# Optimization experiments

Measured on AMD Instinct MI355X. Metric: run time of the kernel, lower is better.

The kernel has to match this reference:

```python
import jax, jax.numpy as jnp
import numpy as np

D = 768
H = 12
DH = 64
S = 1500
SCALE = 0.125  # 1/sqrt(64)


def setup_inputs() -> dict:
    key = jax.random.key(0)
    ks = jax.random.split(key, 8)
    def w(k):
        return jax.random.normal(k, (D, D), dtype=jnp.float32) * (1.0 / np.sqrt(D))
    x = jax.random.normal(ks[0], (8, S, D), dtype=jnp.float32)
    return {
        "x": x,
        "Wq": w(ks[1]), "bq": jax.random.normal(ks[2], (D,), dtype=jnp.float32) * 0.02,
        "Wk": w(ks[3]),
        "Wv": w(ks[4]), "bv": jax.random.normal(ks[5], (D,), dtype=jnp.float32) * 0.02,
        "Wo": w(ks[6]), "bo": jax.random.normal(ks[7], (D,), dtype=jnp.float32) * 0.02,
    }


def reference(x, Wq, bq, Wk, Wv, bv, Wo, bo):
    B = x.shape[0]
    # torch Linear: y = x @ W.T + b
    q = (jnp.einsum('bsd,ed->bse', x, Wq) + bq) * SCALE
    k = jnp.einsum('bsd,ed->bse', x, Wk)
    v = jnp.einsum('bsd,ed->bse', x, Wv) + bv
    # split heads: [B, S, H, DH] -> [B, H, S, DH]
    q = q.reshape(B, S, H, DH).transpose(0, 2, 1, 3)
    k = k.reshape(B, S, H, DH).transpose(0, 2, 1, 3)
    v = v.reshape(B, S, H, DH).transpose(0, 2, 1, 3)
    scores = jnp.einsum('bhqd,bhkd->bhqk', q, k)  # [B, H, S, S]
    probs = jax.nn.softmax(scores, axis=-1)
    ctx = jnp.einsum('bhqk,bhkd->bhqd', probs, v)
    ctx = ctx.transpose(0, 2, 1, 3).reshape(B, S, D)
    return jnp.einsum('bsd,ed->bse', ctx, Wo) + bo
```

## Files before the change

kernel.cpp:

```cpp
#include <hip/hip_runtime.h>
#include <hip/hip_bf16.h>

constexpr int kD  = 768;
constexpr int kH  = 12;
constexpr int kDH = 64;
constexpr int kS  = 1500;
constexpr int kSP = 1504;
constexpr int kB  = 8;
constexpr int kM  = kB * kS;
constexpr float kScale = 0.125f;
constexpr int kPSTR = 72;
constexpr int kNK = kD / 32;

typedef __bf16 bf16;
typedef __bf16 bf16x4 __attribute__((ext_vector_type(4)));
typedef __bf16 bf16x8 __attribute__((ext_vector_type(8)));
typedef float  floatx4 __attribute__((ext_vector_type(4)));

__global__ __launch_bounds__(256) void detect_kernel(const void* __restrict__ xraw,
                                                     int* __restrict__ flag) {
    __shared__ int bad;
    if (threadIdx.x == 0) bad = 0;
    __syncthreads();
    const bf16* xb = (const bf16*)xraw;
    int c = 0;
    for (int k = 0; k < 16; k++) {
        int idx = 2 * (threadIdx.x + 256 * k);
        float v = fabsf((float)xb[idx]);
        if (!(v == 0.0f || (v > 1e-20f && v < 1e6f))) c++;
    }
    atomicAdd(&bad, c);
    __syncthreads();
    if (threadIdx.x == 0) *flag = (bad > 8) ? 1 : 0;
}

__global__ __launch_bounds__(256) void cvt_bf16_kernel(const void* __restrict__ src,
                                                       bf16* __restrict__ dst, int n,
                                                       const int* __restrict__ flag) {
    int i = blockIdx.x * 256 + threadIdx.x;
    if (i < n) {
        if (*flag)
            dst[i] = (bf16)((const float*)src)[i];
        else
            dst[i] = ((const bf16*)src)[i];
    }
}

__global__ __launch_bounds__(256) void cvt_f32_kernel(const void* __restrict__ src,
                                                      float* __restrict__ dst, int n,
                                                      const int* __restrict__ flag) {
    int i = blockIdx.x * 256 + threadIdx.x;
    if (i < n) {
        if (*flag)
            dst[i] = ((const float*)src)[i];
        else
            dst[i] = (float)((const bf16*)src)[i];
    }
}

__global__ __launch_bounds__(256) void zeropad_kernel(bf16* __restrict__ q_ws,
                                                      bf16* __restrict__ k_ws,
                                                      bf16* __restrict__ vt_ws) {
    int t = blockIdx.x * 256 + threadIdx.x;
    if (t < kB * kH * (kSP - kS) * kDH) {
        int bh  = t >> 8;
        int rem = t & 255;
        int s   = kS + (rem >> 6);
        int dh  = rem & 63;
        size_t qi = ((size_t)bh * kSP + s) * kDH + dh;
        q_ws[qi] = (bf16)0.f;
        k_ws[qi] = (bf16)0.f;
        size_t vi = ((size_t)bh * kDH + dh) * kSP + s;
        vt_ws[vi] = (bf16)0.f;
    }
}

__device__ __forceinline__ void async_copy16(const bf16* g, bf16* l) {
    __builtin_amdgcn_global_load_lds(
        (const __attribute__((address_space(1))) void*)g,
        (__attribute__((address_space(3))) void*)l,
        16, 0, 0);
}

#define G_STAGE(KK, SB)                                                         \
    {                                                                           \
        const int k0_ = (KK) * 32;                                              \
        async_copy16(gA + k0_, Asm + (SB) * 4096 + wof);                        \
        async_copy16(gA + (size_t)64 * kD + k0_, Asm + (SB) * 4096 + wof + 2048); \
        async_copy16(gB + k0_, Bsm + (SB) * 4096 + wof);                        \
        async_copy16(gB + (size_t)64 * kD + k0_, Bsm + (SB) * 4096 + wof + 2048); \
    }

#define G_COMPUTE(CB)                                                           \
    {                                                                           \
        const bf16* A_ = Asm + (CB) * 4096;                                     \
        const bf16* B_ = Bsm + (CB) * 4096;                                     \
        bf16x8 af[4], bfr[4];                                                   \
        _Pragma("unroll") for (int i = 0; i < 4; i++)                           \
            af[i] = *(const bf16x8*)(A_ + ((wm + i * 16 + lrow) << 5) + (lq << 3)); \
        _Pragma("unroll") for (int j = 0; j < 4; j++)                           \
            bfr[j] = *(const bf16x8*)(B_ + ((wn + j * 16 + lrow) << 5) + (lq << 3)); \
        _Pragma("unroll") for (int i = 0; i < 4; i++)                           \
            _Pragma("unroll") for (int j = 0; j < 4; j++)                       \
                acc[i][j] = __builtin_amdgcn_mfma_f32_16x16x32_bf16(            \
                    af[i], bfr[j], acc[i][j], 0, 0, 0);                         \
    }

#define G_STEP(KK, CB, SB)                                                      \
    {                                                                           \
        if ((KK) + 3 < kNK) G_STAGE((KK) + 3, SB);                              \
        G_COMPUTE(CB);                                                          \
        if ((KK) + 1 < kNK) {                                                   \
            if ((KK) + 3 < kNK) {                                               \
                asm volatile("s_waitcnt vmcnt(8)" ::: "memory");                \
            } else if ((KK) + 2 < kNK) {                                        \
                asm volatile("s_waitcnt vmcnt(4)" ::: "memory");                \
            } else {                                                            \
                asm volatile("s_waitcnt vmcnt(0)" ::: "memory");                \
            }                                                                   \
            __builtin_amdgcn_s_barrier();                                       \
            __builtin_amdgcn_sched_barrier(0);                                  \
        }                                                                       \
    }

__device__ __forceinline__ void gemm128_qb(const bf16* __restrict__ X,
                                           const bf16* __restrict__ W,
                                           int m0, int n0,
                                           bf16* Asm, bf16* Bsm,
                                           floatx4 acc[4][4]) {
    const int tid  = threadIdx.x;
    const int lane = tid & 63;
    const int w    = tid >> 6;
    const int srow = (w << 4) + (lane >> 2);
    const int scol = (lane & 3) << 3;
    const int lrow = lane & 15;
    const int lq   = lane >> 4;
    const int wm   = (w >> 1) << 6;
    const int wn   = (w & 1) << 6;

    const bf16* gA = X + (size_t)(m0 + srow) * kD + scol;
    const bf16* gB = W + (size_t)(n0 + srow) * kD + scol;
    const int wof = w << 9;

    G_STAGE(0, 0);
    G_STAGE(1, 1);
    G_STAGE(2, 2);
    asm volatile("s_waitcnt vmcnt(8)" ::: "memory");
    __builtin_amdgcn_s_barrier();
    __builtin_amdgcn_sched_barrier(0);

#pragma unroll
    for (int ks = 0; ks < kNK; ks += 4) {
        G_STEP(ks,     0, 3);
        G_STEP(ks + 1, 1, 0);
        G_STEP(ks + 2, 2, 1);
        G_STEP(ks + 3, 3, 2);
    }
}

__global__ __launch_bounds__(256) void qkv_kernel(const bf16* __restrict__ X,
                                                  const bf16* __restrict__ Wq,
                                                  const bf16* __restrict__ Wk,
                                                  const bf16* __restrict__ Wv,
                                                  const float* __restrict__ bq,
                                                  const float* __restrict__ bv,
                                                  bf16* __restrict__ q_ws,
                                                  bf16* __restrict__ k_ws,
                                                  bf16* __restrict__ vt_ws) {
    __shared__ bf16 Asm[4 * 4096];
    __shared__ bf16 Bsm[4 * 4096];

    const int lin = blockIdx.x;
    const int wk  = (lin & 7) * 212 + (lin >> 3);
    if (wk >= 94 * 18) return;
    const int bx  = wk / 18;
    const int r   = wk - bx * 18;
    const int m0  = bx << 7;
    const int mat = r / 6;
    const int n0  = (r % 6) << 7;
    const bf16* W = (mat == 0) ? Wq : (mat == 1) ? Wk : Wv;

    floatx4 acc[4][4] = {};
    gemm128_qb(X, W, m0, n0, Asm, Bsm, acc);

    const int tid  = threadIdx.x;
    const int lane = tid & 63;
    const int w    = tid >> 6;
    const int lrow = lane & 15;
    const int lq   = lane >> 4;
    const int wm   = (w >> 1) << 6;
    const int wn   = (w & 1) << 6;

    if (mat == 2) {
#pragma unroll
        for (int i = 0; i < 4; i++) {
#pragma unroll
            for (int j = 0; j < 4; j++) {
                const int n  = n0 + wn + j * 16 + lrow;
                const int hh = n >> 6, dh = n & 63;
                const float bval = bv[n];
                const int m = m0 + wm + i * 16 + lq * 4;
                if (m >= kM) continue;
                const int bb = m / kS, s = m - bb * kS;
                bf16x4 pv;
#pragma unroll
                for (int r2 = 0; r2 < 4; r2++) pv[r2] = (bf16)(acc[i][j][r2] + bval);
                *(bf16x4*)(vt_ws + (((size_t)(bb * kH + hh)) * kDH + dh) * kSP + s) = pv;
            }
        }
    } else {
        bf16* const dst = (mat == 0) ? q_ws : k_ws;
#pragma unroll
        for (int i = 0; i < 4; i++) {
#pragma unroll
            for (int j = 0; j < 4; j++) {
                const int n  = n0 + wn + j * 16 + lrow;
                const int hh = n >> 6, dh = n & 63;
                const float bval = (mat == 0) ? bq[n] : 0.f;
#pragma unroll
                for (int r2 = 0; r2 < 4; r2++) {
                    const int m = m0 + wm + i * 16 + lq * 4 + r2;
                    if (m >= kM) continue;
                    float v = acc[i][j][r2];
                    if (mat == 0) v = (v + bval) * kScale;
                    const int bb = m / kS, s = m - bb * kS;
                    dst[(((size_t)(bb * kH + hh)) * kSP + s) * kDH + dh] = (bf16)v;
                }
            }
        }
    }
}

__global__ __launch_bounds__(256) void out_kernel(const bf16* __restrict__ X,
                                                  const bf16* __restrict__ Wo,
                                                  const float* __restrict__ bo,
                                                  float* __restrict__ outf) {
    __shared__ bf16 Asm[4 * 4096];
    __shared__ bf16 Bsm[4 * 4096];

    const int m0 = blockIdx.x << 7;
    const int n0 = blockIdx.y << 7;

    floatx4 acc[4][4] = {};
    gemm128_qb(X, Wo, m0, n0, Asm, Bsm, acc);

    const int tid  = threadIdx.x;
    const int lane = tid & 63;
    const int w    = tid >> 6;
    const int lrow = lane & 15;
    const int lq   = lane >> 4;
    const int wm   = (w >> 1) << 6;
    const int wn   = (w & 1) << 6;

#pragma unroll
    for (int i = 0; i < 4; i++) {
#pragma unroll
        for (int j = 0; j < 4; j++) {
            const int n = n0 + wn + j * 16 + lrow;
            const float bval = bo[n];
#pragma unroll
            for (int r = 0; r < 4; r++) {
                const int m = m0 + wm + i * 16 + lq * 4 + r;
                if (m >= kM) continue;
                outf[(size_t)m * kD + n] = acc[i][j][r] + bval;
            }
        }
    }
}

__device__ __forceinline__ const bf16* lds_at(const bf16* sm, int row, int cb) {
    return sm + row * 64 + ((cb ^ ((row & 7) << 4)) >> 1);
}

__device__ __forceinline__ void stage_k(const bf16* __restrict__ kbase, int s0,
                                        bf16* ksm, int w, int lane) {
#pragma unroll
    for (int i = 0; i < 2; i++) {
        const int sidx = i * 4 + w;
        const int row  = sidx * 8 + (lane >> 3);
        const int cb   = (lane & 7) << 4;
        const int scb  = cb ^ ((row & 7) << 4);
        int gr = s0 + row;
        if (gr >= kSP) gr = 1472;
        async_copy16(kbase + (size_t)gr * kDH + (scb >> 1), ksm + sidx * 512);
    }
}

__device__ __forceinline__ void stage_v(const bf16* __restrict__ vbase, int s0,
                                        bf16* vsm, int w, int lane) {
#pragma unroll
    for (int i = 0; i < 2; i++) {
        const int sidx = i * 4 + w;
        const int row  = sidx * 8 + (lane >> 3);
        const int cb   = (lane & 7) << 4;
        const int scb  = cb ^ ((row & 7) << 4);
        int key = s0 + (scb >> 1);
        if (key >= kSP) key = 1472;
        async_copy16(vbase + (size_t)row * kSP + key, vsm + sidx * 512);
    }
}

__device__ __forceinline__ void qk_mfma_lds(const bf16* ksm,
                                            const bf16x8 qf[2][2],
                                            floatx4 sc[2][4],
                                            int col, int quad) {
#pragma unroll
    for (int t = 0; t < 4; t++) {
        const int r = 16 * t + col;
        const bf16x8 kf0 = *(const bf16x8*)lds_at(ksm, r, quad * 16);
        const bf16x8 kf1 = *(const bf16x8*)lds_at(ksm, r, 64 + quad * 16);
        __builtin_amdgcn_s_setprio(1);
#pragma unroll
        for (int qt = 0; qt < 2; qt++) {
            floatx4 a = {0.f, 0.f, 0.f, 0.f};
            a = __builtin_amdgcn_mfma_f32_16x16x32_bf16(kf0, qf[qt][0], a, 0, 0, 0);
            a = __builtin_amdgcn_mfma_f32_16x16x32_bf16(kf1, qf[qt][1], a, 0, 0, 0);
            sc[qt][t] = a;
        }
        __builtin_amdgcn_s_setprio(0);
    }
}

template <bool MASK>
__device__ __forceinline__ void exp_store(const floatx4 sc[2][4],
                                          bf16* __restrict__ Pw,
                                          float lsum[2],
                                          int s0, int col, int quad) {
#pragma unroll
    for (int qt = 0; qt < 2; qt++)
#pragma unroll
        for (int t = 0; t < 4; t++) {
            bf16x4 pv;
#pragma unroll
            for (int r = 0; r < 4; r++) {
                float p;
                if (MASK && (s0 + 16 * t + quad * 4 + r >= kS))
                    p = 0.f;
                else
                    p = __expf(sc[qt][t][r]);
                lsum[qt] += p;
                pv[r] = (bf16)p;
            }
            *(bf16x4*)(Pw + (qt * 16 + col) * kPSTR + 16 * t + quad * 4) = pv;
        }
}

__device__ __forceinline__ void pv_lds(const bf16* vsm,
                                       const bf16* __restrict__ Pr,
                                       floatx4 Oacc[2][4],
                                       int col, int quad) {
    bf16x8 pa[2][2];
#pragma unroll
    for (int qt = 0; qt < 2; qt++)
#pragma unroll
        for (int kc = 0; kc < 2; kc++)
            pa[qt][kc] = *(const bf16x8*)(Pr + (qt * 16 + col) * kPSTR + kc * 32 + quad * 8);
#pragma unroll
    for (int n = 0; n < 4; n++) {
        const int row = n * 16 + col;
#pragma unroll
        for (int kc = 0; kc < 2; kc++) {
            const bf16x8 vf = *(const bf16x8*)lds_at(vsm, row, kc * 64 + quad * 16);
            __builtin_amdgcn_s_setprio(1);
#pragma unroll
            for (int qt = 0; qt < 2; qt++)
                Oacc[qt][n] = __builtin_amdgcn_mfma_f32_16x16x32_bf16(
                    pa[qt][kc], vf, Oacc[qt][n], 0, 0, 0);
            __builtin_amdgcn_s_setprio(0);
        }
    }
}

__global__ __launch_bounds__(256, 2) void fattn_kernel(const bf16* __restrict__ q_ws,
                                                       const bf16* __restrict__ k_ws,
                                                       const bf16* __restrict__ vt_ws,
                                                       bf16* __restrict__ ctx) {
    __shared__ bf16 Ksm[2][64 * 64];
    __shared__ bf16 Vsm[2][64 * 64];
    __shared__ bf16 Pbuf[4][32 * kPSTR];

    const int idx = blockIdx.x;
    const int bh  = idx % 96;
    const int qb  = idx / 96;
    const int b   = bh / kH;
    const int h   = bh - b * kH;
    const int tid  = threadIdx.x;
    const int w    = tid >> 6;
    const int lane = tid & 63;
    const int col  = lane & 15;
    const int quad = lane >> 4;
    const int q0   = qb * 128 + w * 32;
    const bool active = (q0 < kS);

    const bf16* qbase = q_ws  + (size_t)bh * kSP * kDH;
    const bf16* kbase = k_ws  + (size_t)bh * kSP * kDH;
    const bf16* vbase = vt_ws + (size_t)bh * kDH * kSP;

    bf16x8 qf[2][2] = {};
    if (active) {
#pragma unroll
        for (int qt = 0; qt < 2; qt++) {
            const bf16* qr = qbase + (size_t)(q0 + qt * 16 + col) * kDH + quad * 8;
            qf[qt][0] = *(const bf16x8*)(qr);
            qf[qt][1] = *(const bf16x8*)(qr + 32);
        }
    }

    float lsum[2] = {0.f, 0.f};
    floatx4 Oacc[2][4];
#pragma unroll
    for (int qt = 0; qt < 2; qt++)
#pragma unroll
        for (int n = 0; n < 4; n++) Oacc[qt][n] = (floatx4){0.f, 0.f, 0.f, 0.f};

    bf16* const P = &Pbuf[w][0];
    floatx4 sc[2][4];

    stage_k(kbase, 0, &Ksm[0][0], w, lane);
    stage_v(vbase, 0, &Vsm[0][0], w, lane);
    __syncthreads();

    int buf = 0;
    for (int c = 0; c < 23; ++c) {
        stage_k(kbase, (c + 1) * 64, &Ksm[buf ^ 1][0], w, lane);
        stage_v(vbase, (c + 1) * 64, &Vsm[buf ^ 1][0], w, lane);
        if (active) {
            qk_mfma_lds(&Ksm[buf][0], qf, sc, col, quad);
            exp_store<false>(sc, P, lsum, c * 64, col, quad);
            pv_lds(&Vsm[buf][0], P, Oacc, col, quad);
        }
        __syncthreads();
        buf ^= 1;
    }
    if (active) {
        qk_mfma_lds(&Ksm[buf][0], qf, sc, col, quad);
        exp_store<true>(sc, P, lsum, 1472, col, quad);
        pv_lds(&Vsm[buf][0], P, Oacc, col, quad);

#pragma unroll
        for (int qt = 0; qt < 2; qt++) {
            float l = lsum[qt];
            l += __shfl_xor(l, 16);
            l += __shfl_xor(l, 32);
            const float rinv_col = 1.0f / l;
            float ri[4];
#pragma unroll
            for (int r = 0; r < 4; r++)
                ri[r] = __shfl(rinv_col, quad * 4 + r, 16);
#pragma unroll
            for (int n = 0; n < 4; n++)
#pragma unroll
                for (int r = 0; r < 4; r++) {
                    const int q = q0 + qt * 16 + quad * 4 + r;
                    if (q < kS)
                        ctx[((size_t)(b * kS + q)) * kD + h * kDH + n * 16 + col] =
                            (bf16)(Oacc[qt][n][r] * ri[r]);
                }
        }
    }
}

extern "C" void kernel_launch(void* const* d_in, const int* in_sizes, int n_in,
                              void* d_out, int out_size, void* d_ws, size_t ws_size,
                              hipStream_t stream) {
    float* out_f = (float*)d_out;

    constexpr size_t nX = (size_t)kM * kD;
    constexpr size_t nW = (size_t)kD * kD;
    constexpr size_t per_qkv = (size_t)kB * kH * kSP * kDH;

    bf16* xb    = (bf16*)d_ws;
    bf16* Wqb   = xb + nX;
    bf16* Wkb   = Wqb + nW;
    bf16* Wvb   = Wkb + nW;
    bf16* Wob   = Wvb + nW;
    bf16* q_ws  = Wob + nW;
    bf16* k_ws  = q_ws + per_qkv;
    bf16* vt_ws = k_ws + per_qkv;
    float* bqf  = (float*)(vt_ws + per_qkv);
    float* bvf  = bqf + kD;
    float* bof  = bvf + kD;
    int*  flag  = (int*)(bof + kD);
    bf16* ctx   = xb;

    detect_kernel<<<1, 256, 0, stream>>>(d_in[0], flag);
    cvt_bf16_kernel<<<(int)((nX + 255) / 256), 256, 0, stream>>>(d_in[0], xb,  (int)nX, flag);
    cvt_bf16_kernel<<<(int)((nW + 255) / 256), 256, 0, stream>>>(d_in[1], Wqb, (int)nW, flag);
    cvt_bf16_kernel<<<(int)((nW + 255) / 256), 256, 0, stream>>>(d_in[3], Wkb, (int)nW, flag);
    cvt_bf16_kernel<<<(int)((nW + 255) / 256), 256, 0, stream>>>(d_in[4], Wvb, (int)nW, flag);
    cvt_bf16_kernel<<<(int)((nW + 255) / 256), 256, 0, stream>>>(d_in[6], Wob, (int)nW, flag);
    cvt_f32_kernel<<<3, 256, 0, stream>>>(d_in[2], bqf, kD, flag);
    cvt_f32_kernel<<<3, 256, 0, stream>>>(d_in[5], bvf, kD, flag);
    cvt_f32_kernel<<<3, 256, 0, stream>>>(d_in[7], bof, kD, flag);

    zeropad_kernel<<<96, 256, 0, stream>>>(q_ws, k_ws, vt_ws);
    qkv_kernel<<<dim3(1696), 256, 0, stream>>>(xb, Wqb, Wkb, Wvb, bqf, bvf,
                                               q_ws, k_ws, vt_ws);

    fattn_kernel<<<dim3(12 * 96), 256, 0, stream>>>(q_ws, k_ws, vt_ws, ctx);

    dim3 ogrid((kM + 127) / 128, kD / 128);
    out_kernel<<<ogrid, 256, 0, stream>>>(ctx, Wob, bof, out_f);
}
```

Measured before the change: 339.1 us.

## Batch conversion launches, fold log2e into Q scale, remap out GEMM tiles per XCD

```diff
diff --git a/kernel.cpp b/kernel.cpp
--- a/kernel.cpp
+++ b/kernel.cpp
@@ -9,6 +9,7 @@
 constexpr int kB  = 8;
 constexpr int kM  = kB * kS;
 constexpr float kScale = 0.125f;
+constexpr float kScaleL2 = 0.125f * 1.44269504088896f;
 constexpr int kPSTR = 72;
 constexpr int kNK = kD / 32;
 
@@ -46,15 +47,38 @@
     }
 }
 
-__global__ __launch_bounds__(256) void cvt_f32_kernel(const void* __restrict__ src,
-                                                      float* __restrict__ dst, int n,
-                                                      const int* __restrict__ flag) {
+__global__ __launch_bounds__(256) void cvt_w_kernel(const void* __restrict__ s0,
+                                                    const void* __restrict__ s1,
+                                                    const void* __restrict__ s2,
+                                                    const void* __restrict__ s3,
+                                                    bf16* __restrict__ dst, int n,
+                                                    const int* __restrict__ flag) {
+    const int y = blockIdx.y;
+    const void* src = (y == 0) ? s0 : (y == 1) ? s1 : (y == 2) ? s2 : s3;
+    bf16* d = dst + (size_t)y * n;
     int i = blockIdx.x * 256 + threadIdx.x;
     if (i < n) {
         if (*flag)
-            dst[i] = ((const float*)src)[i];
+            d[i] = (bf16)((const float*)src)[i];
         else
-            dst[i] = (float)((const bf16*)src)[i];
+            d[i] = ((const bf16*)src)[i];
+    }
+}
+
+__global__ __launch_bounds__(256) void cvt_b_kernel(const void* __restrict__ s0,
+                                                    const void* __restrict__ s1,
+                                                    const void* __restrict__ s2,
+                                                    float* __restrict__ dst, int n,
+                                                    const int* __restrict__ flag) {
+    const int y = blockIdx.y;
+    const void* src = (y == 0) ? s0 : (y == 1) ? s1 : s2;
+    float* d = dst + (size_t)y * n;
+    int i = blockIdx.x * 256 + threadIdx.x;
+    if (i < n) {
+        if (*flag)
+            d[i] = ((const float*)src)[i];
+        else
+            d[i] = (float)((const bf16*)src)[i];
     }
 }
 
@@ -222,7 +246,7 @@
                     const int m = m0 + wm + i * 16 + lq * 4 + r2;
                     if (m >= kM) continue;
                     float v = acc[i][j][r2];
-                    if (mat == 0) v = (v + bval) * kScale;
+                    if (mat == 0) v = (v + bval) * kScaleL2;
                     const int bb = m / kS, s = m - bb * kS;
                     dst[(((size_t)(bb * kH + hh)) * kSP + s) * kDH + dh] = (bf16)v;
                 }
@@ -238,8 +262,16 @@
     __shared__ bf16 Asm[4 * 4096];
     __shared__ bf16 Bsm[4 * 4096];
 
-    const int m0 = blockIdx.x << 7;
-    const int n0 = blockIdx.y << 7;
+    const int lin = blockIdx.x;
+    const int xcd = lin & 7;
+    const int ii  = lin >> 3;
+    constexpr int q = 564 / 8, r = 564 % 8;
+    if (xcd >= r && ii >= q) return;
+    const int wk = (xcd < r) ? xcd * (q + 1) + ii
+                             : r * (q + 1) + (xcd - r) * q + ii;
+    const int bx = wk / 6;
+    const int m0 = bx << 7;
+    const int n0 = (wk - bx * 6) << 7;
 
     floatx4 acc[4][4] = {};
     gemm128_qb(X, Wo, m0, n0, Asm, Bsm, acc);
@@ -259,10 +291,10 @@
             const int n = n0 + wn + j * 16 + lrow;
             const float bval = bo[n];
 #pragma unroll
-            for (int r = 0; r < 4; r++) {
-                const int m = m0 + wm + i * 16 + lq * 4 + r;
+            for (int r2 = 0; r2 < 4; r2++) {
+                const int m = m0 + wm + i * 16 + lq * 4 + r2;
                 if (m >= kM) continue;
-                outf[(size_t)m * kD + n] = acc[i][j][r] + bval;
+                outf[(size_t)m * kD + n] = acc[i][j][r2] + bval;
             }
         }
     }
@@ -334,10 +366,11 @@
 #pragma unroll
             for (int r = 0; r < 4; r++) {
                 float p;
-                if (MASK && (s0 + 16 * t + quad * 4 + r >= kS))
+                if (MASK && (s0 + 16 * t + quad * 4 + r >= kS)) {
                     p = 0.f;
-                else
-                    p = __expf(sc[qt][t][r]);
+                } else {
+                    asm("v_exp_f32 %0, %1" : "=v"(p) : "v"(sc[qt][t][r]));
+                }
                 lsum[qt] += p;
                 pv[r] = (bf16)p;
             }
@@ -484,14 +517,11 @@
     bf16* ctx   = xb;
 
     detect_kernel<<<1, 256, 0, stream>>>(d_in[0], flag);
-    cvt_bf16_kernel<<<(int)((nX + 255) / 256), 256, 0, stream>>>(d_in[0], xb,  (int)nX, flag);
-    cvt_bf16_kernel<<<(int)((nW + 255) / 256), 256, 0, stream>>>(d_in[1], Wqb, (int)nW, flag);
-    cvt_bf16_kernel<<<(int)((nW + 255) / 256), 256, 0, stream>>>(d_in[3], Wkb, (int)nW, flag);
-    cvt_bf16_kernel<<<(int)((nW + 255) / 256), 256, 0, stream>>>(d_in[4], Wvb, (int)nW, flag);
-    cvt_bf16_kernel<<<(int)((nW + 255) / 256), 256, 0, stream>>>(d_in[6], Wob, (int)nW, flag);
-    cvt_f32_kernel<<<3, 256, 0, stream>>>(d_in[2], bqf, kD, flag);
-    cvt_f32_kernel<<<3, 256, 0, stream>>>(d_in[5], bvf, kD, flag);
-    cvt_f32_kernel<<<3, 256, 0, stream>>>(d_in[7], bof, kD, flag);
+    cvt_bf16_kernel<<<(int)((nX + 255) / 256), 256, 0, stream>>>(d_in[0], xb, (int)nX, flag);
+    cvt_w_kernel<<<dim3((int)((nW + 255) / 256), 4), 256, 0, stream>>>(
+        d_in[1], d_in[3], d_in[4], d_in[6], Wqb, (int)nW, flag);
+    cvt_b_kernel<<<dim3(3, 3), 256, 0, stream>>>(
+        d_in[2], d_in[5], d_in[7], bqf, kD, flag);
 
     zeropad_kernel<<<96, 256, 0, stream>>>(q_ws, k_ws, vt_ws);
     qkv_kernel<<<dim3(1696), 256, 0, stream>>>(xb, Wqb, Wkb, Wvb, bqf, bvf,
@@ -499,6 +529,5 @@
 
     fattn_kernel<<<dim3(12 * 96), 256, 0, stream>>>(q_ws, k_ws, vt_ws, ctx);
 
-    dim3 ogrid((kM + 127) / 128, kD / 128);
-    out_kernel<<<ogrid, 256, 0, stream>>>(ctx, Wob, bof, out_f);
-}
+    out_kernel<<<dim3(568), 256, 0, stream>>>(ctx, Wob, bof, out_f);
+}
```

New measurement: 328.7 us. -3.1%, faster.
